# Performance work log

Hardware: AMD Instinct MI355X
Metric: run time of the kernel (lower is better)

The kernel has to match this reference:

```python
import jax, jax.numpy as jnp
import numpy as np

N, D = 8192, 4096
DIM_K = 4096

def setup_inputs() -> dict:
    key0 = jax.random.key(0)
    k1, k2, k3 = jax.random.split(key0, 3)
    return {
        "query": jax.random.normal(k1, (N, D), dtype=jnp.float32),
        "key": jax.random.normal(k2, (D, N), dtype=jnp.float32),
        "value": jax.random.normal(k3, (N, D), dtype=jnp.float32),
    }

def reference(query, key, value):
    # Faithful to the (buggy) torch module: ELEMENTWISE query * key.T,
    # scale by sqrt(dim_k), elementwise * value, softmax over dim=1
    # (F.softmax's implicit dim for a 2D tensor). The mask branch in the
    # original (`if x:`) cannot execute for multi-element tensors, so it
    # is omitted (mask=None path).
    scale = jnp.sqrt(jnp.float32(DIM_K))
    x = (query * key.T) / scale  # [N, D]
    x = x * value                # [N, D]
    return jax.nn.softmax(x, axis=1)
```

## Files before the change

kernel.cpp:

```cpp
#include <hip/hip_runtime.h>
#include <math.h>


static constexpr int NROW = 8192;
static constexpr int D    = 4096;
static constexpr int RPB  = 16;
static constexpr int TJ   = 256;
static constexpr int NT   = D / TJ;
static constexpr int LSTR = TJ + 4;

#define LDS_BARRIER() asm volatile("s_waitcnt lgkmcnt(0)\n\ts_barrier" ::: "memory")

__global__ __launch_bounds__(1024, 2)
void sdp_softmax_kernel(const float* __restrict__ Q,
                        const float* __restrict__ K,
                        const float* __restrict__ V,
                        float* __restrict__ O)
{
    __shared__ float ldsK[2][RPB * LSTR];

    const int tid  = threadIdx.x;
    const int wv   = tid >> 6;
    const int lane = tid & 63;

    const int nwg = gridDim.x;
    const int cpx = nwg >> 3;
    const int hb  = blockIdx.x;
    const int lb  = (hb & 7) * cpx + (hb >> 3);

    const int row0 = lb * RPB;
    const int r    = row0 + wv;

    const float* qrow = Q + (size_t)r * D;
    const float* vrow = V + (size_t)r * D;
    float*       orow = O + (size_t)r * D;

    const int il = tid & 15;
    const int jg = tid >> 4;
    const float* kbase = K + (size_t)(4 * jg) * NROW + (size_t)row0 + il;

    float ka = kbase[0];
    float kb = kbase[NROW];
    float kc = kbase[2 * (size_t)NROW];
    float kd = kbase[3 * (size_t)NROW];
    *(float4*)&ldsK[0][il * LSTR + 4 * jg] = make_float4(ka, kb, kc, kd);
    {
        const float* p = kbase + (size_t)TJ * NROW;
        ka = p[0]; kb = p[NROW]; kc = p[2 * (size_t)NROW]; kd = p[3 * (size_t)NROW];
    }
    float4 qv = *(const float4*)(qrow + 4 * lane);
    float4 vv = *(const float4*)(vrow + 4 * lane);
    LDS_BARRIER();

    float4 e0, e1, e2, e3, e4, e5, e6, e7,
           e8, e9, e10, e11, e12, e13, e14, e15;
    float s = 0.0f;

#define TILE_ITER(n, EV)                                                      \
    {                                                                         \
        const float4 kf = *(const float4*)&ldsK[(n) & 1][wv * LSTR + 4*lane]; \
        const float4 qc = qv, vc = vv;                                        \
        if ((n) + 1 < NT) {                                                   \
            *(float4*)&ldsK[((n) + 1) & 1][il * LSTR + 4 * jg] =              \
                make_float4(ka, kb, kc, kd);                                  \
            qv = *(const float4*)(qrow + ((n) + 1) * TJ + 4 * lane);          \
            vv = *(const float4*)(vrow + ((n) + 1) * TJ + 4 * lane);          \
        }                                                                     \
        if ((n) + 2 < NT) {                                                   \
            const float* p = kbase + (size_t)((n) + 2) * TJ * NROW;           \
            ka = p[0]; kb = p[NROW];                                          \
            kc = p[2 * (size_t)NROW]; kd = p[3 * (size_t)NROW];               \
        }                                                                     \
        EV.x = __expf(((qc.x * kf.x) * 0.015625f) * vc.x);                    \
        EV.y = __expf(((qc.y * kf.y) * 0.015625f) * vc.y);                    \
        EV.z = __expf(((qc.z * kf.z) * 0.015625f) * vc.z);                    \
        EV.w = __expf(((qc.w * kf.w) * 0.015625f) * vc.w);                    \
        s += (EV.x + EV.y) + (EV.z + EV.w);                                   \
        if ((n) + 1 < NT) LDS_BARRIER();                                      \
        __builtin_amdgcn_sched_barrier(0);                                    \
    }

    TILE_ITER(0,  e0)  TILE_ITER(1,  e1)  TILE_ITER(2,  e2)  TILE_ITER(3,  e3)
    TILE_ITER(4,  e4)  TILE_ITER(5,  e5)  TILE_ITER(6,  e6)  TILE_ITER(7,  e7)
    TILE_ITER(8,  e8)  TILE_ITER(9,  e9)  TILE_ITER(10, e10) TILE_ITER(11, e11)
    TILE_ITER(12, e12) TILE_ITER(13, e13) TILE_ITER(14, e14) TILE_ITER(15, e15)
#undef TILE_ITER

    #pragma unroll
    for (int i = 1; i < 64; i <<= 1)
        s += __shfl_xor(s, i, 64);
    const float inv = 1.0f / s;

#define WRITE_TILE(n, EV)                                                     \
    {                                                                         \
        float4 xx = EV;                                                       \
        xx.x *= inv; xx.y *= inv; xx.z *= inv; xx.w *= inv;                   \
        *(float4*)(orow + (size_t)(n) * TJ + 4 * lane) = xx;                  \
    }

    WRITE_TILE(0,  e0)  WRITE_TILE(1,  e1)  WRITE_TILE(2,  e2)  WRITE_TILE(3,  e3)
    WRITE_TILE(4,  e4)  WRITE_TILE(5,  e5)  WRITE_TILE(6,  e6)  WRITE_TILE(7,  e7)
    WRITE_TILE(8,  e8)  WRITE_TILE(9,  e9)  WRITE_TILE(10, e10) WRITE_TILE(11, e11)
    WRITE_TILE(12, e12) WRITE_TILE(13, e13) WRITE_TILE(14, e14) WRITE_TILE(15, e15)
#undef WRITE_TILE
}

extern "C" void kernel_launch(void* const* d_in, const int* in_sizes, int n_in,
                              void* d_out, int out_size, void* d_ws, size_t ws_size,
                              hipStream_t stream) {
    const float* Q = (const float*)d_in[0];
    const float* K = (const float*)d_in[1];
    const float* V = (const float*)d_in[2];
    float* O = (float*)d_out;

    dim3 grid(NROW / RPB);
    dim3 block(1024);
    sdp_softmax_kernel<<<grid, block, 0, stream>>>(Q, K, V, O);
}
```

Baseline: 118.4 us.

## Double tile width to 512 and rotate register buffers for K/Q/V prefetch

```diff
diff --git a/kernel.cpp b/kernel.cpp
--- a/kernel.cpp
+++ b/kernel.cpp
@@ -5,13 +5,13 @@
 static constexpr int NROW = 8192;
 static constexpr int D    = 4096;
 static constexpr int RPB  = 16;
-static constexpr int TJ   = 256;
+static constexpr int TJ   = 512;
 static constexpr int NT   = D / TJ;
 static constexpr int LSTR = TJ + 4;
 
 #define LDS_BARRIER() asm volatile("s_waitcnt lgkmcnt(0)\n\ts_barrier" ::: "memory")
 
-__global__ __launch_bounds__(1024, 2)
+__global__ __launch_bounds__(1024, 8)
 void sdp_softmax_kernel(const float* __restrict__ Q,
                         const float* __restrict__ K,
                         const float* __restrict__ V,
@@ -37,53 +37,86 @@
 
     const int il = tid & 15;
     const int jg = tid >> 4;
-    const float* kbase = K + (size_t)(4 * jg) * NROW + (size_t)row0 + il;
+    const float* kbase = K + (size_t)(8 * jg) * NROW + (size_t)row0 + il;
+    const float scl = 0.015625f;
 
-    float ka = kbase[0];
-    float kb = kbase[NROW];
-    float kc = kbase[2 * (size_t)NROW];
-    float kd = kbase[3 * (size_t)NROW];
-    *(float4*)&ldsK[0][il * LSTR + 4 * jg] = make_float4(ka, kb, kc, kd);
+    {
+        float t0 = kbase[0];
+        float t1 = kbase[NROW];
+        float t2 = kbase[2 * (size_t)NROW];
+        float t3 = kbase[3 * (size_t)NROW];
+        float t4 = kbase[4 * (size_t)NROW];
+        float t5 = kbase[5 * (size_t)NROW];
+        float t6 = kbase[6 * (size_t)NROW];
+        float t7 = kbase[7 * (size_t)NROW];
+        *(float4*)&ldsK[0][il * LSTR + 8 * jg]     = make_float4(t0, t1, t2, t3);
+        *(float4*)&ldsK[0][il * LSTR + 8 * jg + 4] = make_float4(t4, t5, t6, t7);
+    }
+    float kA0, kA1, kA2, kA3, kA4, kA5, kA6, kA7;
+    float kB0, kB1, kB2, kB3, kB4, kB5, kB6, kB7;
     {
         const float* p = kbase + (size_t)TJ * NROW;
-        ka = p[0]; kb = p[NROW]; kc = p[2 * (size_t)NROW]; kd = p[3 * (size_t)NROW];
+        kA0 = p[0];                  kA1 = p[NROW];
+        kA2 = p[2 * (size_t)NROW];   kA3 = p[3 * (size_t)NROW];
+        kA4 = p[4 * (size_t)NROW];   kA5 = p[5 * (size_t)NROW];
+        kA6 = p[6 * (size_t)NROW];   kA7 = p[7 * (size_t)NROW];
     }
-    float4 qv = *(const float4*)(qrow + 4 * lane);
-    float4 vv = *(const float4*)(vrow + 4 * lane);
+    float4 qA0 = *(const float4*)(qrow + 4 * lane);
+    float4 qA1 = *(const float4*)(qrow + 256 + 4 * lane);
+    float4 vA0 = *(const float4*)(vrow + 4 * lane);
+    float4 vA1 = *(const float4*)(vrow + 256 + 4 * lane);
+    float4 qB0, qB1, vB0, vB1;
     LDS_BARRIER();
 
     float4 e0, e1, e2, e3, e4, e5, e6, e7,
            e8, e9, e10, e11, e12, e13, e14, e15;
     float s = 0.0f;
 
-#define TILE_ITER(n, EV)                                                      \
+#define TILE_ITER(n, EVa, EVb, KW, KL, QC, QN)                                \
     {                                                                         \
-        const float4 kf = *(const float4*)&ldsK[(n) & 1][wv * LSTR + 4*lane]; \
-        const float4 qc = qv, vc = vv;                                        \
-        if ((n) + 1 < NT) {                                                   \
-            *(float4*)&ldsK[((n) + 1) & 1][il * LSTR + 4 * jg] =              \
-                make_float4(ka, kb, kc, kd);                                  \
-            qv = *(const float4*)(qrow + ((n) + 1) * TJ + 4 * lane);          \
-            vv = *(const float4*)(vrow + ((n) + 1) * TJ + 4 * lane);          \
-        }                                                                     \
         if ((n) + 2 < NT) {                                                   \
             const float* p = kbase + (size_t)((n) + 2) * TJ * NROW;           \
-            ka = p[0]; kb = p[NROW];                                          \
-            kc = p[2 * (size_t)NROW]; kd = p[3 * (size_t)NROW];               \
+            KL##0 = p[0];                KL##1 = p[NROW];                     \
+            KL##2 = p[2 * (size_t)NROW]; KL##3 = p[3 * (size_t)NROW];         \
+            KL##4 = p[4 * (size_t)NROW]; KL##5 = p[5 * (size_t)NROW];         \
+            KL##6 = p[6 * (size_t)NROW]; KL##7 = p[7 * (size_t)NROW];         \
         }                                                                     \
-        EV.x = __expf(((qc.x * kf.x) * 0.015625f) * vc.x);                    \
-        EV.y = __expf(((qc.y * kf.y) * 0.015625f) * vc.y);                    \
-        EV.z = __expf(((qc.z * kf.z) * 0.015625f) * vc.z);                    \
-        EV.w = __expf(((qc.w * kf.w) * 0.015625f) * vc.w);                    \
-        s += (EV.x + EV.y) + (EV.z + EV.w);                                   \
+        if ((n) + 1 < NT) {                                                   \
+            q##QN##0 = *(const float4*)(qrow + ((n)+1)*TJ + 4*lane);          \
+            q##QN##1 = *(const float4*)(qrow + ((n)+1)*TJ + 256 + 4*lane);    \
+            v##QN##0 = *(const float4*)(vrow + ((n)+1)*TJ + 4*lane);          \
+            v##QN##1 = *(const float4*)(vrow + ((n)+1)*TJ + 256 + 4*lane);    \
+        }                                                                     \
+        const float4 kf0 = *(const float4*)&ldsK[(n)&1][wv*LSTR + 4*lane];    \
+        const float4 kf1 = *(const float4*)&ldsK[(n)&1][wv*LSTR + 256 + 4*lane];\
+        if ((n) + 1 < NT) {                                                   \
+            *(float4*)&ldsK[((n)+1)&1][il*LSTR + 8*jg] =                      \
+                make_float4(KW##0, KW##1, KW##2, KW##3);                      \
+            *(float4*)&ldsK[((n)+1)&1][il*LSTR + 8*jg + 4] =                  \
+                make_float4(KW##4, KW##5, KW##6, KW##7);                      \
+        }                                                                     \
+        EVa.x = __expf((((q##QC##0).x * kf0.x) * scl) * (v##QC##0).x);        \
+        EVa.y = __expf((((q##QC##0).y * kf0.y) * scl) * (v##QC##0).y);        \
+        EVa.z = __expf((((q##QC##0).z * kf0.z) * scl) * (v##QC##0).z);        \
+        EVa.w = __expf((((q##QC##0).w * kf0.w) * scl) * (v##QC##0).w);        \
+        EVb.x = __expf((((q##QC##1).x * kf1.x) * scl) * (v##QC##1).x);        \
+        EVb.y = __expf((((q##QC##1).y * kf1.y) * scl) * (v##QC##1).y);        \
+        EVb.z = __expf((((q##QC##1).z * kf1.z) * scl) * (v##QC##1).z);        \
+        EVb.w = __expf((((q##QC##1).w * kf1.w) * scl) * (v##QC##1).w);        \
+        s += ((EVa.x + EVa.y) + (EVa.z + EVa.w)) +                            \
+             ((EVb.x + EVb.y) + (EVb.z + EVb.w));                             \
         if ((n) + 1 < NT) LDS_BARRIER();                                      \
         __builtin_amdgcn_sched_barrier(0);                                    \
     }
 
-    TILE_ITER(0,  e0)  TILE_ITER(1,  e1)  TILE_ITER(2,  e2)  TILE_ITER(3,  e3)
-    TILE_ITER(4,  e4)  TILE_ITER(5,  e5)  TILE_ITER(6,  e6)  TILE_ITER(7,  e7)
-    TILE_ITER(8,  e8)  TILE_ITER(9,  e9)  TILE_ITER(10, e10) TILE_ITER(11, e11)
-    TILE_ITER(12, e12) TILE_ITER(13, e13) TILE_ITER(14, e14) TILE_ITER(15, e15)
+    TILE_ITER(0, e0,  e1,  kA, kB, A, B)
+    TILE_ITER(1, e2,  e3,  kB, kA, B, A)
+    TILE_ITER(2, e4,  e5,  kA, kB, A, B)
+    TILE_ITER(3, e6,  e7,  kB, kA, B, A)
+    TILE_ITER(4, e8,  e9,  kA, kB, A, B)
+    TILE_ITER(5, e10, e11, kB, kA, B, A)
+    TILE_ITER(6, e12, e13, kA, kB, A, B)
+    TILE_ITER(7, e14, e15, kB, kA, B, A)
 #undef TILE_ITER
 
     #pragma unroll
@@ -91,11 +124,11 @@
         s += __shfl_xor(s, i, 64);
     const float inv = 1.0f / s;
 
-#define WRITE_TILE(n, EV)                                                     \
+#define WRITE_TILE(c, EV)                                                     \
     {                                                                         \
         float4 xx = EV;                                                       \
         xx.x *= inv; xx.y *= inv; xx.z *= inv; xx.w *= inv;                   \
-        *(float4*)(orow + (size_t)(n) * TJ + 4 * lane) = xx;                  \
+        *(float4*)(orow + (size_t)(c) * 256 + 4 * lane) = xx;                 \
     }
 
     WRITE_TILE(0,  e0)  WRITE_TILE(1,  e1)  WRITE_TILE(2,  e2)  WRITE_TILE(3,  e3)
```

After: 165.9 us. 40.1% more time.

## Stage full K transpose in LDS upfront and drop per-tile barriers

Applied to the files above, without the earlier changes.

```diff
diff --git a/kernel.cpp b/kernel.cpp
--- a/kernel.cpp
+++ b/kernel.cpp
@@ -4,20 +4,19 @@
 
 static constexpr int NROW = 8192;
 static constexpr int D    = 4096;
-static constexpr int RPB  = 16;
-static constexpr int TJ   = 256;
-static constexpr int NT   = D / TJ;
-static constexpr int LSTR = TJ + 4;
+static constexpr int RPB  = 8;
+static constexpr int LSTR = D + 4;
+static constexpr int NT   = 16;
 
 #define LDS_BARRIER() asm volatile("s_waitcnt lgkmcnt(0)\n\ts_barrier" ::: "memory")
 
-__global__ __launch_bounds__(1024, 2)
+__global__ __launch_bounds__(512, 2)
 void sdp_softmax_kernel(const float* __restrict__ Q,
                         const float* __restrict__ K,
                         const float* __restrict__ V,
                         float* __restrict__ O)
 {
-    __shared__ float ldsK[2][RPB * LSTR];
+    __shared__ float ldsK[RPB * LSTR];
 
     const int tid  = threadIdx.x;
     const int wv   = tid >> 6;
@@ -35,67 +34,103 @@
     const float* vrow = V + (size_t)r * D;
     float*       orow = O + (size_t)r * D;
 
-    const int il = tid & 15;
-    const int jg = tid >> 4;
-    const float* kbase = K + (size_t)(4 * jg) * NROW + (size_t)row0 + il;
+    const int il = tid & 7;
+    const int jg = tid >> 3;
+    const float* kbase = K + (size_t)(8 * jg) * NROW + (size_t)row0 + il;
+    const float scl = 0.015625f;
 
-    float ka = kbase[0];
-    float kb = kbase[NROW];
-    float kc = kbase[2 * (size_t)NROW];
-    float kd = kbase[3 * (size_t)NROW];
-    *(float4*)&ldsK[0][il * LSTR + 4 * jg] = make_float4(ka, kb, kc, kd);
-    {
-        const float* p = kbase + (size_t)TJ * NROW;
-        ka = p[0]; kb = p[NROW]; kc = p[2 * (size_t)NROW]; kd = p[3 * (size_t)NROW];
+    float sa0, sa1, sa2, sa3, sa4, sa5, sa6, sa7;
+    float sb0, sb1, sb2, sb3, sb4, sb5, sb6, sb7;
+
+#define LOADB(R, b)                                                           \
+    {                                                                         \
+        const float* p = kbase + (size_t)(512 * (b)) * NROW;                  \
+        R##0 = p[0];                  R##1 = p[NROW];                         \
+        R##2 = p[2 * (size_t)NROW];   R##3 = p[3 * (size_t)NROW];             \
+        R##4 = p[4 * (size_t)NROW];   R##5 = p[5 * (size_t)NROW];             \
+        R##6 = p[6 * (size_t)NROW];   R##7 = p[7 * (size_t)NROW];             \
     }
-    float4 qv = *(const float4*)(qrow + 4 * lane);
-    float4 vv = *(const float4*)(vrow + 4 * lane);
+#define WRITEB(R, b)                                                          \
+    {                                                                         \
+        float* w = &ldsK[il * LSTR + 512 * (b) + 8 * jg];                     \
+        *(float4*)w       = make_float4(R##0, R##1, R##2, R##3);              \
+        *(float4*)(w + 4) = make_float4(R##4, R##5, R##6, R##7);              \
+    }
+
+    LOADB(sa, 0)
+    float4 qS0 = *(const float4*)(qrow + 0 * 256 + 4 * lane);
+    float4 vS0 = *(const float4*)(vrow + 0 * 256 + 4 * lane);
+    float4 qS1 = *(const float4*)(qrow + 1 * 256 + 4 * lane);
+    float4 vS1 = *(const float4*)(vrow + 1 * 256 + 4 * lane);
+    float4 qS2 = *(const float4*)(qrow + 2 * 256 + 4 * lane);
+    float4 vS2 = *(const float4*)(vrow + 2 * 256 + 4 * lane);
+    float4 qS3 = *(const float4*)(qrow + 3 * 256 + 4 * lane);
+    float4 vS3 = *(const float4*)(vrow + 3 * 256 + 4 * lane);
+
+    LOADB(sb, 1) WRITEB(sa, 0)
+    LOADB(sa, 2) WRITEB(sb, 1)
+    LOADB(sb, 3) WRITEB(sa, 2)
+    LOADB(sa, 4) WRITEB(sb, 3)
+    LOADB(sb, 5) WRITEB(sa, 4)
+    LOADB(sa, 6) WRITEB(sb, 5)
+    LOADB(sb, 7) WRITEB(sa, 6)
+    WRITEB(sb, 7)
+#undef LOADB
+#undef WRITEB
+
     LDS_BARRIER();
 
+    float4 kfA = *(const float4*)&ldsK[wv * LSTR + 4 * lane];
+    float4 kfB;
     float4 e0, e1, e2, e3, e4, e5, e6, e7,
            e8, e9, e10, e11, e12, e13, e14, e15;
     float s = 0.0f;
 
-#define TILE_ITER(n, EV)                                                      \
+#define BODY(t, ET, KC, KN, QS, VS)                                           \
     {                                                                         \
-        const float4 kf = *(const float4*)&ldsK[(n) & 1][wv * LSTR + 4*lane]; \
-        const float4 qc = qv, vc = vv;                                        \
-        if ((n) + 1 < NT) {                                                   \
-            *(float4*)&ldsK[((n) + 1) & 1][il * LSTR + 4 * jg] =              \
-                make_float4(ka, kb, kc, kd);                                  \
-            qv = *(const float4*)(qrow + ((n) + 1) * TJ + 4 * lane);          \
-            vv = *(const float4*)(vrow + ((n) + 1) * TJ + 4 * lane);          \
+        if ((t) + 1 < NT)                                                     \
+            KN = *(const float4*)&ldsK[wv * LSTR + ((t) + 1) * 256 + 4*lane]; \
+        const float4 qc = QS, vc = VS;                                        \
+        if ((t) + 4 < NT) {                                                   \
+            QS = *(const float4*)(qrow + ((t) + 4) * 256 + 4 * lane);         \
+            VS = *(const float4*)(vrow + ((t) + 4) * 256 + 4 * lane);         \
         }                                                                     \
-        if ((n) + 2 < NT) {                                                   \
-            const float* p = kbase + (size_t)((n) + 2) * TJ * NROW;           \
-            ka = p[0]; kb = p[NROW];                                          \
-            kc = p[2 * (size_t)NROW]; kd = p[3 * (size_t)NROW];               \
-        }                                                                     \
-        EV.x = __expf(((qc.x * kf.x) * 0.015625f) * vc.x);                    \
-        EV.y = __expf(((qc.y * kf.y) * 0.015625f) * vc.y);                    \
-        EV.z = __expf(((qc.z * kf.z) * 0.015625f) * vc.z);                    \
-        EV.w = __expf(((qc.w * kf.w) * 0.015625f) * vc.w);                    \
-        s += (EV.x + EV.y) + (EV.z + EV.w);                                   \
-        if ((n) + 1 < NT) LDS_BARRIER();                                      \
+        ET.x = __expf(((qc.x * (KC).x) * scl) * vc.x);                        \
+        ET.y = __expf(((qc.y * (KC).y) * scl) * vc.y);                        \
+        ET.z = __expf(((qc.z * (KC).z) * scl) * vc.z);                        \
+        ET.w = __expf(((qc.w * (KC).w) * scl) * vc.w);                        \
+        s += ((ET.x + ET.y) + (ET.z + ET.w));                                 \
         __builtin_amdgcn_sched_barrier(0);                                    \
     }
 
-    TILE_ITER(0,  e0)  TILE_ITER(1,  e1)  TILE_ITER(2,  e2)  TILE_ITER(3,  e3)
-    TILE_ITER(4,  e4)  TILE_ITER(5,  e5)  TILE_ITER(6,  e6)  TILE_ITER(7,  e7)
-    TILE_ITER(8,  e8)  TILE_ITER(9,  e9)  TILE_ITER(10, e10) TILE_ITER(11, e11)
-    TILE_ITER(12, e12) TILE_ITER(13, e13) TILE_ITER(14, e14) TILE_ITER(15, e15)
-#undef TILE_ITER
+    BODY(0,  e0,  kfA, kfB, qS0, vS0)
+    BODY(1,  e1,  kfB, kfA, qS1, vS1)
+    BODY(2,  e2,  kfA, kfB, qS2, vS2)
+    BODY(3,  e3,  kfB, kfA, qS3, vS3)
+    BODY(4,  e4,  kfA, kfB, qS0, vS0)
+    BODY(5,  e5,  kfB, kfA, qS1, vS1)
+    BODY(6,  e6,  kfA, kfB, qS2, vS2)
+    BODY(7,  e7,  kfB, kfA, qS3, vS3)
+    BODY(8,  e8,  kfA, kfB, qS0, vS0)
+    BODY(9,  e9,  kfB, kfA, qS1, vS1)
+    BODY(10, e10, kfA, kfB, qS2, vS2)
+    BODY(11, e11, kfB, kfA, qS3, vS3)
+    BODY(12, e12, kfA, kfB, qS0, vS0)
+    BODY(13, e13, kfB, kfA, qS1, vS1)
+    BODY(14, e14, kfA, kfB, qS2, vS2)
+    BODY(15, e15, kfB, kfA, qS3, vS3)
+#undef BODY
 
     #pragma unroll
     for (int i = 1; i < 64; i <<= 1)
         s += __shfl_xor(s, i, 64);
     const float inv = 1.0f / s;
 
-#define WRITE_TILE(n, EV)                                                     \
+#define WRITE_TILE(t, ET)                                                     \
     {                                                                         \
-        float4 xx = EV;                                                       \
+        float4 xx = ET;                                                       \
         xx.x *= inv; xx.y *= inv; xx.z *= inv; xx.w *= inv;                   \
-        *(float4*)(orow + (size_t)(n) * TJ + 4 * lane) = xx;                  \
+        *(float4*)(orow + (size_t)(t) * 256 + 4 * lane) = xx;                 \
     }
 
     WRITE_TILE(0,  e0)  WRITE_TILE(1,  e1)  WRITE_TILE(2,  e2)  WRITE_TILE(3,  e3)
@@ -114,6 +149,6 @@
     float* O = (float*)d_out;
 
     dim3 grid(NROW / RPB);
-    dim3 block(1024);
+    dim3 block(512);
     sdp_softmax_kernel<<<grid, block, 0, stream>>>(Q, K, V, O);
 }
```

Measured after the change: 121.3 us. +2.5%, slower.
